# Kernel optimization log

Hardware: AMD Instinct MI355X
Metric: run time of the kernel (lower is better)

Reference implementation:

```python
import jax, jax.numpy as jnp
import numpy as np


def _rx(state, theta, axis):
    # Apply RX(theta) to qubit at tensor axis `axis`. state: (B, 2,...,2) complex.
    half = theta * 0.5
    c = jnp.cos(half)
    s = jnp.sin(half)
    a0 = jnp.take(state, 0, axis=axis)
    a1 = jnp.take(state, 1, axis=axis)
    return jnp.stack([c * a0 - 1j * s * a1, c * a1 - 1j * s * a0], axis=axis)


def _cnot(state, w):
    # CNOT with control wire w (axis w+1), target wire w+1 (axis w+2).
    c_ax = w + 1
    s0 = jnp.take(state, 0, axis=c_ax)
    # after removing the control axis, the target axis index becomes c_ax
    s1 = jnp.flip(jnp.take(state, 1, axis=c_ax), axis=c_ax)
    return jnp.stack([s0, s1], axis=c_ax)


def _run_circuit(x, params):
    # x: (B, n) encoding angles; params: (depth, n) trainable RX angles.
    B, n = x.shape
    depth = params.shape[0]
    state = jnp.zeros((B,) + (2,) * n, jnp.complex64)
    state = state.at[(slice(None),) + (0,) * n].set(1.0 + 0.0j)
    # angle encoding: RX(x_w) on each wire
    for w in range(n):
        theta = x[:, w].reshape((B,) + (1,) * (n - 1))
        state = _rx(state, theta, w + 1)
    # variational layers: RX(param) per wire, then CNOT chain
    for d in range(depth):
        for w in range(n):
            state = _rx(state, params[d, w], w + 1)
        for w in range(n - 1):
            state = _cnot(state, w)
    probs = state.real ** 2 + state.imag ** 2  # (B, 2,...,2)
    ez = []
    for w in range(n):
        axes = tuple(a for a in range(1, n + 1) if a != w + 1)
        p = probs.sum(axes)  # (B, 2)
        ez.append(p[:, 0] - p[:, 1])  # <Z_w>
    return jnp.stack(ez, axis=1)  # (B, n)


def setup_inputs() -> dict:
    key = jax.random.key(0)
    k0, k1, k2, k3, k4 = jax.random.split(key, 5)
    seq_len, batch, input_dim = 256, 128, 64
    n_qubits, depth, hidden = 10, 2, 256
    inputs = jax.random.normal(k0, (seq_len, batch, input_dim), jnp.float32)
    mask = jax.random.randint(k1, (seq_len, batch), 0, 2).astype(jnp.int32)
    qparams = jax.random.normal(k2, (4, depth, n_qubits), jnp.float32)
    W = jax.random.normal(k3, (4, hidden, n_qubits), jnp.float32) / np.sqrt(n_qubits)
    b = jax.random.normal(k4, (4, hidden), jnp.float32) * 0.01
    return {"inputs": inputs, "mask": mask, "qparams": qparams, "W": W, "b": b}


def reference(inputs, mask, qparams, W, b):
    seq_len, batch, _ = inputs.shape
    n = qparams.shape[-1]
    hidden = W.shape[1]
    maskf = mask.astype(inputs.dtype)

    circuits4 = jax.vmap(_run_circuit, in_axes=(None, 0))  # over the 4 gates

    def step(carry, xm):
        hx, cx = carry
        x_t, m_t = xm
        q_in = jnp.concatenate([x_t, hx], axis=1)[:, :n]  # (B, n)
        z = circuits4(q_in, qparams)                      # (4, B, n)
        pre = jnp.einsum('gbn,ghn->gbh', z, W) + b[:, None, :]
        f = jax.nn.sigmoid(pre[0])
        i = jax.nn.sigmoid(pre[1])
        g = jnp.tanh(pre[2])
        o = jax.nn.sigmoid(pre[3])
        m = m_t[:, None]
        f = f * m + (1.0 - m)
        i = i * m
        g = g * m
        o = o * m + (1.0 - m)
        cx_new = f * cx + i * g
        hx_new = o * jnp.tanh(cx_new)
        return (hx_new, cx_new), hx_new

    h0 = jnp.zeros((batch, hidden), inputs.dtype)
    c0 = jnp.zeros((batch, hidden), inputs.dtype)
    (hx, cx), outputs = jax.lax.scan(jax.checkpoint(step), (h0, c0), (inputs, maskf))
    return outputs, (hx, cx)
```

## Files before the change

### kernel.cpp

```cpp
#include <hip/hip_runtime.h>

#define T_LEN 256
#define BATCH 128
#define NQ 10
#define HID 256
#define OUT_HX (T_LEN * BATCH * HID)
#define OUT_CX (OUT_HX + BATCH * HID)

#define KS  (-1.44269504089f)
#define KT2 (-2.88539008178f)

__global__ __launch_bounds__(256) void zker(
    const float* __restrict__ inputs,
    const float* __restrict__ qparams,
    float* __restrict__ zws)
{
  const int b   = blockIdx.x;
  const int tq  = blockIdx.y;
  const int tid = threadIdx.x;
  const int t   = tq * 64 + (tid >> 2);
  const int g   = tid & 3;

  const float sg = (g == 2) ? KT2 : KS;

  float th0[NQ], cth[NQ], sth[NQ];
#pragma unroll
  for (int k = 0; k < NQ; ++k) {
    th0[k]   = qparams[g * 2 * NQ + k];
    float t1 = qparams[g * 2 * NQ + NQ + k];
    sth[k] = __sinf(t1);
    cth[k] = __cosf(t1);
  }
  float cphi[NQ], sphi[NQ];
  const float* xp = inputs + (t * BATCH + b) * 64;
#pragma unroll
  for (int k = 0; k < NQ; ++k) {
    float ang = xp[k] + th0[k];
    sphi[k] = __sinf(ang);
    cphi[k] = __cosf(ang);
  }
  float* zout = zws + (b * T_LEN + t) * 40 + g;
#pragma unroll
  for (int w = 0; w < NQ; ++w) {
    float vI, vZ, vY, vX; int js;
    if (w == NQ - 1) { vI = 0.f; vZ = cth[NQ-1]; vY = sth[NQ-1]; vX = 0.f; js = NQ - 2; }
    else             { vI = 1.f; vZ = 0.f; vY = 0.f; vX = 0.f; js = w; }
#pragma unroll
    for (int j = js; j >= 0; --j) {
      float nI = cth[j] * (cphi[j+1] * vZ - sphi[j+1] * vY);
      float nZ = cth[j] * vI;
      float nY = sth[j] * vX;
      float nX = -sth[j] * (sphi[j+1] * vZ + cphi[j+1] * vY);
      vI = nI; vZ = nZ; vY = nY; vX = nX;
    }
    zout[w * 4] = (vI + cphi[0] * vZ - sphi[0] * vY) * sg;
  }
}

__global__ __launch_bounds__(512, 4) void scanker(
    const float* __restrict__ zws,
    const int*  __restrict__ mask,
    const float* __restrict__ W,
    const float* __restrict__ bias,
    float* __restrict__ out)
{
  const int b    = blockIdx.x;
  const int h0   = blockIdx.y * 64;
  const int tid  = threadIdx.x;
  const int lane = tid & 63;
  const int wavu = __builtin_amdgcn_readfirstlane(tid >> 6);
  const int h    = h0 + lane;

  __shared__ float mk[T_LEN];
  __shared__ float cA[8][64];
  __shared__ float cW[8][64];

  for (int t = tid; t < T_LEN; t += 512) mk[t] = (float)mask[t * BATCH + b];

  float Wf[NQ], Wi[NQ], Wg[NQ], Wo[NQ];
#pragma unroll
  for (int n = 0; n < NQ; ++n) {
    Wf[n] = W[(0 * HID + h) * NQ + n];
    Wi[n] = W[(1 * HID + h) * NQ + n];
    Wg[n] = W[(2 * HID + h) * NQ + n];
    Wo[n] = W[(3 * HID + h) * NQ + n];
  }
  const float bf = bias[0 * HID + h] * KS;
  const float bi = bias[1 * HID + h] * KS;
  const float bg = bias[2 * HID + h] * KT2;
  const float bo = bias[3 * HID + h] * KS;

  const float* zb = zws + b * T_LEN * 40;
  __syncthreads();

  float av[32], wv[32];
  float A = 1.f, Wc = 0.f;
#pragma unroll
  for (int k = 0; k < 32; ++k) {
    const int t = wavu * 32 + k;
    const float* zr = zb + t * 40;
    const float m = mk[t];
    const float onem = 1.f - m;
    float p0 = bf, p1 = bi, p2 = bg;
#pragma unroll
    for (int n = 0; n < NQ; ++n) {
      p0 = fmaf(zr[n * 4 + 0], Wf[n], p0);
      p1 = fmaf(zr[n * 4 + 1], Wi[n], p1);
      p2 = fmaf(zr[n * 4 + 2], Wg[n], p2);
    }
    const float uf = __builtin_amdgcn_rcpf(1.f + __builtin_amdgcn_exp2f(p0));
    const float ui = __builtin_amdgcn_rcpf(1.f + __builtin_amdgcn_exp2f(p1));
    const float ug = __builtin_amdgcn_rcpf(1.f + __builtin_amdgcn_exp2f(p2));
    const float a  = fmaf(m, uf, onem);
    const float wt = m * ui * fmaf(2.f, ug, -1.f);
    av[k] = a;
    wv[k] = wt;
    Wc = fmaf(a, Wc, wt);
    A  = a * A;
  }
  cA[wavu][lane] = A;
  cW[wavu][lane] = Wc;
  __syncthreads();

  float c = 0.f;
  for (int k = 0; k < wavu; ++k)
    c = fmaf(cA[k][lane], c, cW[k][lane]);

  float hv = 0.f;
#pragma unroll
  for (int k = 0; k < 32; ++k) {
    const int t = wavu * 32 + k;
    const float* zr = zb + t * 40;
    const float m = mk[t];
    float p3 = bo;
#pragma unroll
    for (int n = 0; n < NQ; ++n)
      p3 = fmaf(zr[n * 4 + 3], Wo[n], p3);
    const float uo = __builtin_amdgcn_rcpf(1.f + __builtin_amdgcn_exp2f(p3));
    const float om = fmaf(m, uo, 1.f - m);
    c = fmaf(av[k], c, wv[k]);
    const float ec = __builtin_amdgcn_exp2f(c * KT2);
    const float tc = fmaf(2.f, __builtin_amdgcn_rcpf(1.f + ec), -1.f);
    hv = om * tc;
    out[t * (BATCH * HID) + b * HID + h] = hv;
  }
  if (wavu == 7) {
    out[OUT_HX + b * HID + h] = hv;
    out[OUT_CX + b * HID + h] = c;
  }
}

extern "C" void kernel_launch(void* const* d_in, const int* in_sizes, int n_in,
                              void* d_out, int out_size, void* d_ws, size_t ws_size,
                              hipStream_t stream)
{
  int ii = 0, im = 1, iq = 2, iw = 3, ib = 4;
  for (int i = 0; i < n_in; ++i) {
    switch (in_sizes[i]) {
      case 2097152: ii = i; break;
      case 32768:   im = i; break;
      case 80:      iq = i; break;
      case 10240:   iw = i; break;
      case 1024:    ib = i; break;
      default: break;
    }
  }
  const float* inputs  = (const float*)d_in[ii];
  const int*   mask    = (const int*)d_in[im];
  const float* qparams = (const float*)d_in[iq];
  const float* W       = (const float*)d_in[iw];
  const float* bias    = (const float*)d_in[ib];
  float*       out     = (float*)d_out;
  float*       zws     = (float*)d_ws;

  zker<<<dim3(BATCH, 4), dim3(256), 0, stream>>>(inputs, qparams, zws);
  scanker<<<dim3(BATCH, 4), dim3(512), 0, stream>>>(zws, mask, W, bias, out);
}
```

Before: 117.0 us.

## Skip masked timesteps in scan, vectorize z loads, recompute forget gate

The scan kernel now branches on the mask per timestep. Masked steps skip the gate dot products and transcendentals and reuse the previous tanh(c) as the output. The z rows are read as float4, the shared-memory mask staging and its barrier are removed, and the per-step forget coefficient is recomputed in the second pass instead of being held in a 32-entry register array. This lowers register pressure (launch bounds relaxed to 2) and wasted work, in exchange for some recomputation and divergence, since the mask varies per batch and the branch is uniform per block.

```diff
diff --git a/kernel.cpp b/kernel.cpp
--- a/kernel.cpp
+++ b/kernel.cpp
@@ -57,7 +57,7 @@
   }
 }
 
-__global__ __launch_bounds__(512, 4) void scanker(
+__global__ __launch_bounds__(512, 2) void scanker(
     const float* __restrict__ zws,
     const int*  __restrict__ mask,
     const float* __restrict__ W,
@@ -71,11 +71,8 @@
   const int wavu = __builtin_amdgcn_readfirstlane(tid >> 6);
   const int h    = h0 + lane;
 
-  __shared__ float mk[T_LEN];
   __shared__ float cA[8][64];
   __shared__ float cW[8][64];
-
-  for (int t = tid; t < T_LEN; t += 512) mk[t] = (float)mask[t * BATCH + b];
 
   float Wf[NQ], Wi[NQ], Wg[NQ], Wo[NQ];
 #pragma unroll
@@ -91,32 +88,32 @@
   const float bo = bias[3 * HID + h] * KS;
 
   const float* zb = zws + b * T_LEN * 40;
-  __syncthreads();
 
-  float av[32], wv[32];
+  float wv[32];
   float A = 1.f, Wc = 0.f;
 #pragma unroll
   for (int k = 0; k < 32; ++k) {
     const int t = wavu * 32 + k;
-    const float* zr = zb + t * 40;
-    const float m = mk[t];
-    const float onem = 1.f - m;
-    float p0 = bf, p1 = bi, p2 = bg;
+    if (mask[t * BATCH + b]) {
+      const float4* zrow = (const float4*)(zb + t * 40);
+      float p0 = bf, p1 = bi, p2 = bg;
 #pragma unroll
-    for (int n = 0; n < NQ; ++n) {
-      p0 = fmaf(zr[n * 4 + 0], Wf[n], p0);
-      p1 = fmaf(zr[n * 4 + 1], Wi[n], p1);
-      p2 = fmaf(zr[n * 4 + 2], Wg[n], p2);
+      for (int n = 0; n < NQ; ++n) {
+        const float4 z = zrow[n];
+        p0 = fmaf(z.x, Wf[n], p0);
+        p1 = fmaf(z.y, Wi[n], p1);
+        p2 = fmaf(z.z, Wg[n], p2);
+      }
+      const float a  = __builtin_amdgcn_rcpf(1.f + __builtin_amdgcn_exp2f(p0));
+      const float ui = __builtin_amdgcn_rcpf(1.f + __builtin_amdgcn_exp2f(p1));
+      const float ug = __builtin_amdgcn_rcpf(1.f + __builtin_amdgcn_exp2f(p2));
+      const float wt = ui * fmaf(2.f, ug, -1.f);
+      wv[k] = wt;
+      Wc = fmaf(a, Wc, wt);
+      A  = a * A;
+    } else {
+      wv[k] = 0.f;
     }
-    const float uf = __builtin_amdgcn_rcpf(1.f + __builtin_amdgcn_exp2f(p0));
-    const float ui = __builtin_amdgcn_rcpf(1.f + __builtin_amdgcn_exp2f(p1));
-    const float ug = __builtin_amdgcn_rcpf(1.f + __builtin_amdgcn_exp2f(p2));
-    const float a  = fmaf(m, uf, onem);
-    const float wt = m * ui * fmaf(2.f, ug, -1.f);
-    av[k] = a;
-    wv[k] = wt;
-    Wc = fmaf(a, Wc, wt);
-    A  = a * A;
   }
   cA[wavu][lane] = A;
   cW[wavu][lane] = Wc;
@@ -126,22 +123,34 @@
   for (int k = 0; k < wavu; ++k)
     c = fmaf(cA[k][lane], c, cW[k][lane]);
 
-  float hv = 0.f;
+  float tc;
+  {
+    const float ec = __builtin_amdgcn_exp2f(c * KT2);
+    tc = fmaf(2.f, __builtin_amdgcn_rcpf(1.f + ec), -1.f);
+  }
+
+  float hv = tc;
 #pragma unroll
   for (int k = 0; k < 32; ++k) {
     const int t = wavu * 32 + k;
-    const float* zr = zb + t * 40;
-    const float m = mk[t];
-    float p3 = bo;
+    if (mask[t * BATCH + b]) {
+      const float4* zrow = (const float4*)(zb + t * 40);
+      float p0 = bf, p3 = bo;
 #pragma unroll
-    for (int n = 0; n < NQ; ++n)
-      p3 = fmaf(zr[n * 4 + 3], Wo[n], p3);
-    const float uo = __builtin_amdgcn_rcpf(1.f + __builtin_amdgcn_exp2f(p3));
-    const float om = fmaf(m, uo, 1.f - m);
-    c = fmaf(av[k], c, wv[k]);
-    const float ec = __builtin_amdgcn_exp2f(c * KT2);
-    const float tc = fmaf(2.f, __builtin_amdgcn_rcpf(1.f + ec), -1.f);
-    hv = om * tc;
+      for (int n = 0; n < NQ; ++n) {
+        const float4 z = zrow[n];
+        p0 = fmaf(z.x, Wf[n], p0);
+        p3 = fmaf(z.w, Wo[n], p3);
+      }
+      const float a  = __builtin_amdgcn_rcpf(1.f + __builtin_amdgcn_exp2f(p0));
+      const float uo = __builtin_amdgcn_rcpf(1.f + __builtin_amdgcn_exp2f(p3));
+      c = fmaf(a, c, wv[k]);
+      const float ec = __builtin_amdgcn_exp2f(c * KT2);
+      tc = fmaf(2.f, __builtin_amdgcn_rcpf(1.f + ec), -1.f);
+      hv = uo * tc;
+    } else {
+      hv = tc;
+    }
     out[t * (BATCH * HID) + b * HID + h] = hv;
   }
   if (wavu == 7) {
```

After: 116.6 us. About the same (-0.4%).
